# Optimization experiments

Measured on AMD Instinct MI355X. Metric: run time of the kernel, lower is better.

Reference implementation:

```python
import jax, jax.numpy as jnp
import numpy as np

B, T, OBS, H, A, S = 4096, 64, 64, 64, 8, 201


def setup_inputs() -> dict:
    key = jax.random.key(0)
    ks = jax.random.split(key, 13)
    n = lambda k, shp, s=1.0: jax.random.normal(k, shp, dtype=jnp.float32) * s
    return {
        "x": n(ks[0], (B, T, OBS)),
        "stack": jnp.zeros((B, S, H), jnp.float32),
        "stack_ptrs": jax.random.randint(ks[1], (B, 1), 0, 100, dtype=jnp.int32),
        # core_network: init.normal_(std=1.0) per source
        "W1": n(ks[2], (H, OBS + H)), "b1": n(ks[3], (H,)),
        "W2": n(ks[4], (H, H)), "b2": n(ks[5], (H,)),
        # stack_head: default torch Linear init ~ U(-1/sqrt(H), 1/sqrt(H))
        "Ws": (jax.random.uniform(ks[6], (3, H), dtype=jnp.float32) * 2 - 1) / np.sqrt(H),
        "bs": (jax.random.uniform(ks[7], (3,), dtype=jnp.float32) * 2 - 1) / np.sqrt(H),
        # policy/value heads: init.normal_(std=0.01)
        "Wp": n(ks[8], (A, H), 0.01), "bp": n(ks[9], (A,), 0.01),
        "Wv": n(ks[10], (1, H), 0.01), "bv": n(ks[11], (1,), 0.01),
    }


def reference(x, stack, stack_ptrs, W1, b1, W2, b2, Ws, bs, Wp, bp, Wv, bv):
    # x: [B,T,OBS]  stack: [B,S,H]  stack_ptrs: [B,1] int
    batch = x.shape[0]
    bidx = jnp.arange(batch)
    ptrs0 = stack_ptrs.astype(jnp.int32)[:, 0]  # [B]

    def step(carry, x_t):
        stk, ptrs = carry
        top = stk[bidx, ptrs]                                   # [B,H] gather at ptr
        h = jnp.tanh(jnp.concatenate([x_t, top], axis=1) @ W1.T + b1)
        p = jnp.tanh(h @ W2.T + b2)                             # [B,H]
        probs = jax.nn.softmax(p @ Ws.T + bs, axis=1)           # [B,3]
        ops = jnp.argmax(probs, axis=1).astype(jnp.int32)       # 0=pop,1=noop,2=push
        push = (ops == 2)[:, None]
        # conditional scatter: write p at row ptr only where op==2
        stk = stk.at[bidx, ptrs].set(jnp.where(push, p, top))
        ptrs = jnp.maximum(ptrs + ops - 1, 0)
        logits = p @ Wp.T + bp                                  # [B,A]
        value = (p @ Wv.T + bv)[:, 0]                           # [B]
        return (stk, ptrs), (logits, value)

    (stack_out, ptrs_out), (logits_t, values_t) = jax.lax.scan(
        step, (stack, ptrs0), jnp.swapaxes(x, 0, 1))
    logitss = jnp.swapaxes(logits_t, 0, 1)      # [B,T,A]
    values = values_t.reshape(-1)               # time-major [T*B], matching torch layout
    return logitss, values, stack_out, ptrs_out[:, None]
```

## Files before the change

### kernel.cpp

```cpp
#include <hip/hip_runtime.h>
#include <cstddef>

#define NB 4096
#define NT 64
#define NOBS 64
#define NH 64
#define NA 8
#define NS 201


__device__ __forceinline__ float bl(float v, int k) {
    return __int_as_float(__builtin_amdgcn_readlane(__float_as_int(v), k));
}

__device__ __forceinline__ float chain64(const float* __restrict__ w,
                                         float vec, float acc) {
#pragma unroll
    for (int c = 0; c < 4; ++c) {
        float sb[16];
#pragma unroll
        for (int j = 0; j < 16; ++j) sb[j] = bl(vec, 16 * c + j);
#pragma unroll
        for (int j = 0; j < 16; ++j)
            acc = fmaf(w[16 * c + j], sb[j], acc);
    }
    return acc;
}

__launch_bounds__(64, 2)
__global__ void stacknet_kernel(const float* __restrict__ x,
                                const float* __restrict__ stack_in,
                                const int* __restrict__ ptrs_in,
                                const float* __restrict__ W1,
                                const float* __restrict__ b1,
                                const float* __restrict__ W2,
                                const float* __restrict__ b2,
                                const float* __restrict__ Ws,
                                const float* __restrict__ bs,
                                const float* __restrict__ Wp,
                                const float* __restrict__ bp,
                                const float* __restrict__ Wv,
                                const float* __restrict__ bv,
                                float* __restrict__ logits_out,
                                float* __restrict__ values_out,
                                float* __restrict__ stack,
                                float* __restrict__ ptrs_out) {
    const int lane = threadIdx.x;
    const int b    = blockIdx.x;
    const int aa   = lane & 15;

    __shared__ float xcl[NT * NH];

    const float* xb = x + (size_t)b * NT * NOBS;
    float* stk      = stack + (size_t)b * NS * NH;

    {
        const float4* s4 = (const float4*)(stack_in + (size_t)b * (NS * NH));
        float4* d4 = (float4*)stk;
#pragma unroll 4
        for (int i = lane; i < (NS * NH / 4); i += 64) d4[i] = s4[i];
    }

    {
        float w1x[64];
#pragma unroll
        for (int j = 0; j < 16; ++j) {
            float4 w = ((const float4*)W1)[lane * 32 + j];
            w1x[4*j] = w.x; w1x[4*j+1] = w.y; w1x[4*j+2] = w.z; w1x[4*j+3] = w.w;
        }
        float xv = xb[lane];
#pragma unroll 1
        for (int t = 0; t < NT; ++t) {
            float xnext = (t + 1 < NT) ? xb[(t + 1) * 64 + lane] : 0.f;
            xcl[t * 64 + lane] = chain64(w1x, xv, 0.f);
            xv = xnext;
        }
    }

    float w1h[64], w2r[64], hw[64];
#pragma unroll
    for (int j = 0; j < 16; ++j) {
        float4 wa = ((const float4*)W1)[lane * 32 + 16 + j];
        w1h[4*j] = wa.x; w1h[4*j+1] = wa.y; w1h[4*j+2] = wa.z; w1h[4*j+3] = wa.w;
        float4 wb = ((const float4*)W2)[lane * 16 + j];
        w2r[4*j] = wb.x; w2r[4*j+1] = wb.y; w2r[4*j+2] = wb.z; w2r[4*j+3] = wb.w;
    }
    if (aa < 12) {
        const float* hsrc = (aa < 3) ? (Ws + aa * 64)
                          : (aa < 11) ? (Wp + (aa - 3) * 64) : Wv;
#pragma unroll
        for (int j = 0; j < 16; ++j) {
            float4 w = *(const float4*)(hsrc + 4 * j);
            hw[4*j] = w.x; hw[4*j+1] = w.y; hw[4*j+2] = w.z; hw[4*j+3] = w.w;
        }
    } else {
#pragma unroll
        for (int k = 0; k < 64; ++k) hw[k] = 0.f;
    }
    float b1r  = b1[lane];
    float b2r  = b2[lane];
    float shba = (aa < 3) ? bs[aa] : (aa < 11) ? bp[aa - 3] : (aa == 11) ? bv[0] : 0.f;

    asm volatile("s_waitcnt vmcnt(0)" ::: "memory");

    int ptr   = ptrs_in[b];
    float top = stk[ptr * 64 + lane];
    int   lastRow = -1, lastRow2 = -1;
    float lastVal = 0.f, lastVal2 = 0.f;

    float* lgb = logits_out + (size_t)b * NT * NA;

    int r0    = (ptr > 0) ? (ptr - 1) : 0;
    float c0  = stk[r0 * 64 + lane];
    float c2  = stk[(ptr + 1) * 64 + lane];
    float xcv = xcl[lane];

#pragma unroll 1
    for (int t = 0; t < NT; ++t) {
        float h = tanhf(chain64(w1h, top, xcv) + b1r);

        float p = tanhf(chain64(w2r, h, 0.f) + b2r);

        float sv = chain64(hw, p, 0.f) + shba;

        float s0 = bl(sv, 0), s1 = bl(sv, 1), s2 = bl(sv, 2);
        float mx = fmaxf(fmaxf(s0, s1), s2);
        float e0 = expf(s0 - mx), e1 = expf(s1 - mx), e2 = expf(s2 - mx);
        float S = (e0 + e1) + e2;
        float q0 = e0 / S, q1 = e1 / S, q2 = e2 / S;
        int op = 0; float pm = q0;
        if (q1 > pm) { pm = q1; op = 1; }
        if (q2 > pm) { op = 2; }

        int np = ptr + op - 1;
        np = (np < 0) ? 0 : np;

        int nr0 = (np > 0) ? (np - 1) : 0;
        float nc0 = stk[nr0 * 64 + lane];
        float nc2 = stk[(np + 1) * 64 + lane];
        int tn = (t + 1 < NT) ? (t + 1) : t;
        float nxcv = xcl[tn * 64 + lane];

        if (op == 2) stk[ptr * 64 + lane] = p;

        float sel;
        if (op == 0) {
            sel = (r0 == lastRow) ? lastVal
                : (r0 == lastRow2) ? lastVal2 : c0;
        } else if (op == 1) {
            sel = top;
        } else {
            int r2 = ptr + 1;
            sel = (r2 == lastRow) ? lastVal
                : (r2 == lastRow2) ? lastVal2 : c2;
        }
        if (op == 2) { lastRow2 = lastRow; lastVal2 = lastVal;
                       lastRow = ptr;      lastVal  = p; }

        ptr = np;
        top = sel;
        r0  = nr0;
        c0  = nc0;
        c2  = nc2;
        xcv = nxcv;

        if (lane >= 3 && lane <= 10) lgb[t * NA + (lane - 3)] = sv;
        if (lane == 11) values_out[(size_t)t * NB + b] = sv;
    }
    if (lane == 0) ptrs_out[b] = (float)ptr;
}

extern "C" void kernel_launch(void* const* d_in, const int* in_sizes, int n_in,
                              void* d_out, int out_size, void* d_ws, size_t ws_size,
                              hipStream_t stream) {
    const float* x        = (const float*)d_in[0];
    const float* stack_in = (const float*)d_in[1];
    const int*   ptrs_in  = (const int*)d_in[2];
    const float* W1 = (const float*)d_in[3];
    const float* b1 = (const float*)d_in[4];
    const float* W2 = (const float*)d_in[5];
    const float* b2 = (const float*)d_in[6];
    const float* Ws = (const float*)d_in[7];
    const float* bs = (const float*)d_in[8];
    const float* Wp = (const float*)d_in[9];
    const float* bp = (const float*)d_in[10];
    const float* Wv = (const float*)d_in[11];
    const float* bv = (const float*)d_in[12];

    float* out      = (float*)d_out;
    float* logits   = out;
    float* values   = out + 2097152;
    float* stack    = out + 2359296;
    float* ptrs_out = out + 55050240;

    stacknet_kernel<<<NB, 64, 0, stream>>>(x, stack_in, ptrs_in,
                                           W1, b1, W2, b2, Ws, bs,
                                           Wp, bp, Wv, bv,
                                           logits, values, stack, ptrs_out);
}
```

Measured before the change: 763.9 us.

## Process two batch rows per wavefront with LDS vector broadcast instead of readlane

Each 64-lane block now runs the recurrence for two batch elements at once, interleaving their FMA chains so the two independent dependency chains hide each other's latency. Vector broadcasts go through shared-memory float4 reads instead of per-element readlane. Half the LDS holds the precomputed x projections, and the other half is parked in unused stack rows 164-195, which are restored from stack_in after the loop. This halves the grid and adds register pressure, and it relies on the pointer never reaching those parked rows during the scan.

```diff
diff --git a/kernel.cpp b/kernel.cpp
--- a/kernel.cpp
+++ b/kernel.cpp
@@ -21,8 +21,7 @@
 #pragma unroll
         for (int j = 0; j < 16; ++j) sb[j] = bl(vec, 16 * c + j);
 #pragma unroll
-        for (int j = 0; j < 16; ++j)
-            acc = fmaf(w[16 * c + j], sb[j], acc);
+        for (int j = 0; j < 16; ++j) acc = fmaf(w[16 * c + j], sb[j], acc);
     }
     return acc;
 }
@@ -46,19 +45,30 @@
                                 float* __restrict__ stack,
                                 float* __restrict__ ptrs_out) {
     const int lane = threadIdx.x;
-    const int b    = blockIdx.x;
+    const int jb0  = blockIdx.x * 2;
+    const int jb1  = jb0 + 1;
     const int aa   = lane & 15;
 
-    __shared__ float xcl[NT * NH];
-
-    const float* xb = x + (size_t)b * NT * NOBS;
-    float* stk      = stack + (size_t)b * NS * NH;
+    __shared__ float xcl0[32 * NH];
+    __shared__ float xcl1[32 * NH];
+    __shared__ __align__(16) float vb0[192];
+    __shared__ __align__(16) float vb1[192];
+
+    const float* xb0 = x + (size_t)jb0 * NT * NOBS;
+    const float* xb1 = x + (size_t)jb1 * NT * NOBS;
+    float* stk0 = stack + (size_t)jb0 * NS * NH;
+    float* stk1 = stack + (size_t)jb1 * NS * NH;
 
     {
-        const float4* s4 = (const float4*)(stack_in + (size_t)b * (NS * NH));
-        float4* d4 = (float4*)stk;
+        const float4* s40 = (const float4*)(stack_in + (size_t)jb0 * NS * NH);
+        const float4* s41 = (const float4*)(stack_in + (size_t)jb1 * NS * NH);
+        float4* d40 = (float4*)stk0;
+        float4* d41 = (float4*)stk1;
 #pragma unroll 4
-        for (int i = lane; i < (NS * NH / 4); i += 64) d4[i] = s4[i];
+        for (int i = lane; i < 164 * 16; i += 64) { d40[i] = s40[i]; d41[i] = s41[i]; }
+        for (int i = lane; i < 80; i += 64) {
+            d40[3136 + i] = s40[3136 + i]; d41[3136 + i] = s41[3136 + i];
+        }
     }
 
     {
@@ -68,12 +78,21 @@
             float4 w = ((const float4*)W1)[lane * 32 + j];
             w1x[4*j] = w.x; w1x[4*j+1] = w.y; w1x[4*j+2] = w.z; w1x[4*j+3] = w.w;
         }
-        float xv = xb[lane];
+        float xv0 = xb0[lane], xv1 = xb1[lane];
 #pragma unroll 1
         for (int t = 0; t < NT; ++t) {
-            float xnext = (t + 1 < NT) ? xb[(t + 1) * 64 + lane] : 0.f;
-            xcl[t * 64 + lane] = chain64(w1x, xv, 0.f);
-            xv = xnext;
+            float xn0 = (t + 1 < NT) ? xb0[(t + 1) * 64 + lane] : 0.f;
+            float xn1 = (t + 1 < NT) ? xb1[(t + 1) * 64 + lane] : 0.f;
+            float a0 = chain64(w1x, xv0, 0.f);
+            float a1 = chain64(w1x, xv1, 0.f);
+            if (t < 32) {
+                xcl0[t * 64 + lane] = a0;
+                xcl1[t * 64 + lane] = a1;
+            } else {
+                stk0[(132 + t) * 64 + lane] = a0;
+                stk1[(132 + t) * 64 + lane] = a1;
+            }
+            xv0 = xn0; xv1 = xn1;
         }
     }
 
@@ -103,71 +122,160 @@
 
     asm volatile("s_waitcnt vmcnt(0)" ::: "memory");
 
-    int ptr   = ptrs_in[b];
-    float top = stk[ptr * 64 + lane];
-    int   lastRow = -1, lastRow2 = -1;
-    float lastVal = 0.f, lastVal2 = 0.f;
-
-    float* lgb = logits_out + (size_t)b * NT * NA;
-
-    int r0    = (ptr > 0) ? (ptr - 1) : 0;
-    float c0  = stk[r0 * 64 + lane];
-    float c2  = stk[(ptr + 1) * 64 + lane];
-    float xcv = xcl[lane];
+    int ptr0 = ptrs_in[jb0], ptr1 = ptrs_in[jb1];
+    float top0 = stk0[ptr0 * 64 + lane];
+    float top1 = stk1[ptr1 * 64 + lane];
+    int   lA0 = -1, lA0b = -1, lA1 = -1, lA1b = -1;
+    float lV0 = 0.f, lV0b = 0.f, lV1 = 0.f, lV1b = 0.f;
+
+    float* lgb0 = logits_out + (size_t)jb0 * NT * NA;
+    float* lgb1 = logits_out + (size_t)jb1 * NT * NA;
+
+    int r00 = (ptr0 > 0) ? (ptr0 - 1) : 0;
+    int r01 = (ptr1 > 0) ? (ptr1 - 1) : 0;
+    float c00 = stk0[r00 * 64 + lane], c20 = stk0[(ptr0 + 1) * 64 + lane];
+    float c01 = stk1[r01 * 64 + lane], c21 = stk1[(ptr1 + 1) * 64 + lane];
+    float xcv0 = xcl0[lane], xcv1 = xcl1[lane];
 
 #pragma unroll 1
     for (int t = 0; t < NT; ++t) {
-        float h = tanhf(chain64(w1h, top, xcv) + b1r);
-
-        float p = tanhf(chain64(w2r, h, 0.f) + b2r);
-
-        float sv = chain64(hw, p, 0.f) + shba;
-
-        float s0 = bl(sv, 0), s1 = bl(sv, 1), s2 = bl(sv, 2);
-        float mx = fmaxf(fmaxf(s0, s1), s2);
-        float e0 = expf(s0 - mx), e1 = expf(s1 - mx), e2 = expf(s2 - mx);
-        float S = (e0 + e1) + e2;
-        float q0 = e0 / S, q1 = e1 / S, q2 = e2 / S;
-        int op = 0; float pm = q0;
-        if (q1 > pm) { pm = q1; op = 1; }
-        if (q2 > pm) { op = 2; }
-
-        int np = ptr + op - 1;
-        np = (np < 0) ? 0 : np;
-
-        int nr0 = (np > 0) ? (np - 1) : 0;
-        float nc0 = stk[nr0 * 64 + lane];
-        float nc2 = stk[(np + 1) * 64 + lane];
-        int tn = (t + 1 < NT) ? (t + 1) : t;
-        float nxcv = xcl[tn * 64 + lane];
-
-        if (op == 2) stk[ptr * 64 + lane] = p;
-
-        float sel;
-        if (op == 0) {
-            sel = (r0 == lastRow) ? lastVal
-                : (r0 == lastRow2) ? lastVal2 : c0;
-        } else if (op == 1) {
-            sel = top;
+        vb0[lane] = top0;
+        vb1[lane] = top1;
+        float acc0 = xcv0, acc1 = xcv1;
+        {
+            const float4* v40 = (const float4*)vb0;
+            const float4* v41 = (const float4*)vb1;
+#pragma unroll
+            for (int j = 0; j < 16; ++j) {
+                float4 a0 = v40[j], a1 = v41[j];
+                acc0 = fmaf(w1h[4*j],   a0.x, acc0); acc1 = fmaf(w1h[4*j],   a1.x, acc1);
+                acc0 = fmaf(w1h[4*j+1], a0.y, acc0); acc1 = fmaf(w1h[4*j+1], a1.y, acc1);
+                acc0 = fmaf(w1h[4*j+2], a0.z, acc0); acc1 = fmaf(w1h[4*j+2], a1.z, acc1);
+                acc0 = fmaf(w1h[4*j+3], a0.w, acc0); acc1 = fmaf(w1h[4*j+3], a1.w, acc1);
+            }
+        }
+        float h0 = tanhf(acc0 + b1r), h1 = tanhf(acc1 + b1r);
+
+        vb0[64 + lane] = h0;
+        vb1[64 + lane] = h1;
+        float ac20 = 0.f, ac21 = 0.f;
+        {
+            const float4* h40 = (const float4*)(vb0 + 64);
+            const float4* h41 = (const float4*)(vb1 + 64);
+#pragma unroll
+            for (int j = 0; j < 16; ++j) {
+                float4 a0 = h40[j], a1 = h41[j];
+                ac20 = fmaf(w2r[4*j],   a0.x, ac20); ac21 = fmaf(w2r[4*j],   a1.x, ac21);
+                ac20 = fmaf(w2r[4*j+1], a0.y, ac20); ac21 = fmaf(w2r[4*j+1], a1.y, ac21);
+                ac20 = fmaf(w2r[4*j+2], a0.z, ac20); ac21 = fmaf(w2r[4*j+2], a1.z, ac21);
+                ac20 = fmaf(w2r[4*j+3], a0.w, ac20); ac21 = fmaf(w2r[4*j+3], a1.w, ac21);
+            }
+        }
+        float p0 = tanhf(ac20 + b2r), p1 = tanhf(ac21 + b2r);
+
+        vb0[128 + lane] = p0;
+        vb1[128 + lane] = p1;
+        float hc0 = 0.f, hc1 = 0.f;
+        {
+            const float4* p40 = (const float4*)(vb0 + 128);
+            const float4* p41 = (const float4*)(vb1 + 128);
+#pragma unroll
+            for (int j = 0; j < 16; ++j) {
+                float4 a0 = p40[j], a1 = p41[j];
+                hc0 = fmaf(a0.x, hw[4*j],   hc0); hc1 = fmaf(a1.x, hw[4*j],   hc1);
+                hc0 = fmaf(a0.y, hw[4*j+1], hc0); hc1 = fmaf(a1.y, hw[4*j+1], hc1);
+                hc0 = fmaf(a0.z, hw[4*j+2], hc0); hc1 = fmaf(a1.z, hw[4*j+2], hc1);
+                hc0 = fmaf(a0.w, hw[4*j+3], hc0); hc1 = fmaf(a1.w, hw[4*j+3], hc1);
+            }
+        }
+        float sv0 = hc0 + shba, sv1 = hc1 + shba;
+
+        int op0, op1;
+        {
+            float s0 = bl(sv0, 0), s1 = bl(sv0, 1), s2 = bl(sv0, 2);
+            float mx = fmaxf(fmaxf(s0, s1), s2);
+            float e0 = expf(s0 - mx), e1 = expf(s1 - mx), e2 = expf(s2 - mx);
+            float S = (e0 + e1) + e2;
+            float q0 = e0 / S, q1 = e1 / S, q2 = e2 / S;
+            op0 = 0; float pm = q0;
+            if (q1 > pm) { pm = q1; op0 = 1; }
+            if (q2 > pm) { op0 = 2; }
+        }
+        {
+            float s0 = bl(sv1, 0), s1 = bl(sv1, 1), s2 = bl(sv1, 2);
+            float mx = fmaxf(fmaxf(s0, s1), s2);
+            float e0 = expf(s0 - mx), e1 = expf(s1 - mx), e2 = expf(s2 - mx);
+            float S = (e0 + e1) + e2;
+            float q0 = e0 / S, q1 = e1 / S, q2 = e2 / S;
+            op1 = 0; float pm = q0;
+            if (q1 > pm) { pm = q1; op1 = 1; }
+            if (q2 > pm) { op1 = 2; }
+        }
+
+        int np0 = ptr0 + op0 - 1; np0 = (np0 < 0) ? 0 : np0;
+        int np1 = ptr1 + op1 - 1; np1 = (np1 < 0) ? 0 : np1;
+
+        int nr00 = (np0 > 0) ? (np0 - 1) : 0;
+        int nr01 = (np1 > 0) ? (np1 - 1) : 0;
+        float nc00 = stk0[nr00 * 64 + lane];
+        float nc20 = stk0[(np0 + 1) * 64 + lane];
+        float nc01 = stk1[nr01 * 64 + lane];
+        float nc21 = stk1[(np1 + 1) * 64 + lane];
+        int tn = t + 1;
+        float nxcv0, nxcv1;
+        if (tn < 32) {
+            nxcv0 = xcl0[tn * 64 + lane];
+            nxcv1 = xcl1[tn * 64 + lane];
         } else {
-            int r2 = ptr + 1;
-            sel = (r2 == lastRow) ? lastVal
-                : (r2 == lastRow2) ? lastVal2 : c2;
-        }
-        if (op == 2) { lastRow2 = lastRow; lastVal2 = lastVal;
-                       lastRow = ptr;      lastVal  = p; }
-
-        ptr = np;
-        top = sel;
-        r0  = nr0;
-        c0  = nc0;
-        c2  = nc2;
-        xcv = nxcv;
-
-        if (lane >= 3 && lane <= 10) lgb[t * NA + (lane - 3)] = sv;
-        if (lane == 11) values_out[(size_t)t * NB + b] = sv;
-    }
-    if (lane == 0) ptrs_out[b] = (float)ptr;
+            nxcv0 = stk0[(132 + tn) * 64 + lane];
+            nxcv1 = stk1[(132 + tn) * 64 + lane];
+        }
+
+        if (op0 == 2) stk0[ptr0 * 64 + lane] = p0;
+        if (op1 == 2) stk1[ptr1 * 64 + lane] = p1;
+
+        float sel0;
+        if (op0 == 0)      sel0 = (r00 == lA0) ? lV0 : (r00 == lA0b) ? lV0b : c00;
+        else if (op0 == 1) sel0 = top0;
+        else { int r2 = ptr0 + 1;
+               sel0 = (r2 == lA0) ? lV0 : (r2 == lA0b) ? lV0b : c20; }
+        if (op0 == 2) { lA0b = lA0; lV0b = lV0; lA0 = ptr0; lV0 = p0; }
+
+        float sel1;
+        if (op1 == 0)      sel1 = (r01 == lA1) ? lV1 : (r01 == lA1b) ? lV1b : c01;
+        else if (op1 == 1) sel1 = top1;
+        else { int r2 = ptr1 + 1;
+               sel1 = (r2 == lA1) ? lV1 : (r2 == lA1b) ? lV1b : c21; }
+        if (op1 == 2) { lA1b = lA1; lV1b = lV1; lA1 = ptr1; lV1 = p1; }
+
+        ptr0 = np0; top0 = sel0; r00 = nr00; c00 = nc00; c20 = nc20; xcv0 = nxcv0;
+        ptr1 = np1; top1 = sel1; r01 = nr01; c01 = nc01; c21 = nc21; xcv1 = nxcv1;
+
+        if (lane >= 3 && lane <= 10) {
+            lgb0[t * NA + (lane - 3)] = sv0;
+            lgb1[t * NA + (lane - 3)] = sv1;
+        }
+        if (lane == 11) {
+            values_out[(size_t)t * NB + jb0] = sv0;
+            values_out[(size_t)t * NB + jb1] = sv1;
+        }
+    }
+    if (lane == 0) {
+        ptrs_out[jb0] = (float)ptr0;
+        ptrs_out[jb1] = (float)ptr1;
+    }
+
+    {
+        const float4* s40 = (const float4*)(stack_in + (size_t)jb0 * NS * NH);
+        const float4* s41 = (const float4*)(stack_in + (size_t)jb1 * NS * NH);
+        float4* d40 = (float4*)stk0;
+        float4* d41 = (float4*)stk1;
+#pragma unroll
+        for (int i = lane; i < 32 * 16; i += 64) {
+            d40[2624 + i] = s40[2624 + i];
+            d41[2624 + i] = s41[2624 + i];
+        }
+    }
 }
 
 extern "C" void kernel_launch(void* const* d_in, const int* in_sizes, int n_in,
@@ -193,8 +301,8 @@
     float* stack    = out + 2359296;
     float* ptrs_out = out + 55050240;
 
-    stacknet_kernel<<<NB, 64, 0, stream>>>(x, stack_in, ptrs_in,
-                                           W1, b1, W2, b2, Ws, bs,
-                                           Wp, bp, Wv, bv,
-                                           logits, values, stack, ptrs_out);
+    stacknet_kernel<<<NB / 2, 64, 0, stream>>>(x, stack_in, ptrs_in,
+                                               W1, b1, W2, b2, Ws, bs,
+                                               Wp, bp, Wv, bv,
+                                               logits, values, stack, ptrs_out);
 }
```

After: 1.474 ms. 92.9% more time.
